# Optimization experiments

Measured on AMD Instinct MI355X. Metric: run time of the kernel, lower is better.

Reference implementation:

```python
import jax, jax.numpy as jnp
import numpy as np

N_POINTS = 1048576
N_LEVELS = 16
F = 2
BASE_RES = 16
FINEST_RES = 512
LOG2_HASH = 19
SIZES = [2 ** min(i + 1, LOG2_HASH) for i in range(N_LEVELS)]  # per-level table rows (powers of 2)
OFFS = np.concatenate([[0], np.cumsum(SIZES)]).astype(np.int64)  # static row offsets into packed table
TOTAL_ROWS = int(OFFS[-1])  # 131070
# hash primes from the torch module; uint32 wraparound matches int64 low-bit behavior
# because each table size is a power of two <= 2^19 < 2^32, so h % 2^k == low k bits.
P0, P1, P2, P3 = np.uint32(1), np.uint32(2654435761), np.uint32(29675113), np.uint32(123456789)
CORNERS = np.array([[0,0,0],[1,0,0],[0,1,0],[1,1,0],
                    [0,0,1],[1,0,1],[0,1,1],[1,1,1]], dtype=np.uint32)  # torch stacking order


def setup_inputs() -> dict:
    key = jax.random.key(0)
    k1, k2 = jax.random.split(key)
    coords = jax.random.uniform(k1, (N_POINTS, 3), dtype=jnp.float32, minval=-1.0, maxval=1.0)
    hash_init_scale = 0.001
    table = jax.random.uniform(k2, (TOTAL_ROWS, F), dtype=jnp.float32,
                               minval=-hash_init_scale, maxval=hash_init_scale)
    return {"coords": coords, "table": table}


def _encode(coords, table):
    corners = jnp.asarray(CORNERS)  # [8,3] uint32
    outs = []
    for level in range(N_LEVELS):
        res = min(BASE_RES * (2 ** level), FINEST_RES)
        cs = (coords + 1.0) * res           # [N,3]
        cf = jnp.floor(cs)
        frac = cs - cf                      # [N,3]
        base = cf.astype(jnp.uint32)        # coords >= -1 so floor >= 0
        c = base[None, :, :] + corners[:, None, :]   # [8,N,3]
        x, y, z = c[..., 0], c[..., 1], c[..., 2]
        h = x * P0
        h = h * P1 + y
        h = h * P2 + z
        h = h * P3
        h = (h & jnp.uint32(SIZES[level] - 1)).astype(jnp.int32)  # mod power-of-2 table size
        feats = table[int(OFFS[level]) + h]          # [8,N,F] gather
        tx = frac[..., 0:1]; ty = frac[..., 1:2]; tz = frac[..., 2:3]
        f = (feats[0] * (1 - tx) * (1 - ty) * (1 - tz)
             + feats[1] * tx * (1 - ty) * (1 - tz)
             + feats[2] * (1 - tx) * ty * (1 - tz)
             + feats[3] * tx * ty * (1 - tz)
             + feats[4] * (1 - tx) * (1 - ty) * tz
             + feats[5] * tx * (1 - ty) * tz
             + feats[6] * (1 - tx) * ty * tz
             + feats[7] * tx * ty * tz)              # [N,F]
        outs.append(f)
    return jnp.concatenate(outs, axis=-1)            # [N, N_LEVELS*F]


def reference(coords, table):
    return _encode(coords, table)
```

## Files before the change

### kernel.cpp

```cpp
#include <hip/hip_runtime.h>
#include <hip/hip_fp16.h>


#define N_POINTS 1048576
#define BLOCK 1024
#define STAGED_ROWS 16382
#define STAGED_BYTES (STAGED_ROWS * 4)

__device__ __forceinline__ float2 ldsRow(const unsigned* __restrict__ lds, unsigned idx) {
    unsigned u = lds[idx];
    __half2 h = *(__half2*)&u;
    return __half22float2(h);
}

__global__ __launch_bounds__(BLOCK, 8) void ngp_encode_kernel(
    const float* __restrict__ coords,
    const float* __restrict__ table,
    float* __restrict__ out)
{
    extern __shared__ unsigned lds_tb[];

    {
        const float4* __restrict__ t4 = (const float4*)table;
        uint2* __restrict__ l2 = (uint2*)lds_tb;
        const int n = STAGED_ROWS / 2;
        for (int r = threadIdx.x; r < n; r += BLOCK) {
            float4 v = t4[r];
            __half2 a = __floats2half2_rn(v.x, v.y);
            __half2 b = __floats2half2_rn(v.z, v.w);
            uint2 u;
            u.x = *(unsigned*)&a;
            u.y = *(unsigned*)&b;
            l2[r] = u;
        }
    }
    __syncthreads();

    const int i = blockIdx.x * BLOCK + threadIdx.x;

    const float px = coords[3 * i + 0];
    const float py = coords[3 * i + 1];
    const float pz = coords[3 * i + 2];

    constexpr unsigned P1 = 2654435761u, P2 = 29675113u, P3 = 123456789u;
    constexpr unsigned HA = P1 * P2 * P3;
    constexpr unsigned HB = P2 * P3;
    constexpr unsigned HC = P3;
    const unsigned D[8] = {0u, HA, HB, HA + HB, HC, HA + HC, HB + HC, HA + HB + HC};

    const float2* __restrict__ tb = (const float2*)table;

    float res_out[32];

#pragma unroll
    for (int l = 0; l < 5; ++l) {
        const float fres = (float)(16 << l);
        const float csx = (px + 1.0f) * fres;
        const float csy = (py + 1.0f) * fres;
        const float csz = (pz + 1.0f) * fres;
        const float cfx = floorf(csx), cfy = floorf(csy), cfz = floorf(csz);
        const float tx = csx - cfx, ty = csy - cfy, tz = csz - cfz;
        const unsigned h000 = (unsigned)cfx * HA + (unsigned)cfy * HB + (unsigned)cfz * HC;
        const float ux = 1.0f - tx, uy = 1.0f - ty, uz = 1.0f - tz;
        const float w[8] = {ux*uy*uz, tx*uy*uz, ux*ty*uz, tx*ty*uz,
                            ux*uy*tz, tx*uy*tz, ux*ty*tz, tx*ty*tz};
        const unsigned mask = (2u << l) - 1u;
        const unsigned off  = (2u << l) - 2u;
        float o0 = 0.0f, o1 = 0.0f;
#pragma unroll
        for (int c = 0; c < 8; ++c) {
            float2 f = ldsRow(lds_tb, off + ((h000 + D[c]) & mask));
            o0 += f.x * w[c];
            o1 += f.y * w[c];
        }
        res_out[2 * l + 0] = o0;
        res_out[2 * l + 1] = o1;
    }

    float w5[8];
    unsigned H[8];
    {
        const float fres = 512.0f;
        const float csx = (px + 1.0f) * fres;
        const float csy = (py + 1.0f) * fres;
        const float csz = (pz + 1.0f) * fres;
        const float cfx = floorf(csx), cfy = floorf(csy), cfz = floorf(csz);
        const float tx = csx - cfx, ty = csy - cfy, tz = csz - cfz;
        const unsigned h000 = (unsigned)cfx * HA + (unsigned)cfy * HB + (unsigned)cfz * HC;
        const float ux = 1.0f - tx, uy = 1.0f - ty, uz = 1.0f - tz;
        w5[0] = ux*uy*uz; w5[1] = tx*uy*uz; w5[2] = ux*ty*uz; w5[3] = tx*ty*uz;
        w5[4] = ux*uy*tz; w5[5] = tx*uy*tz; w5[6] = ux*ty*tz; w5[7] = tx*ty*tz;
#pragma unroll
        for (int c = 0; c < 8; ++c) H[c] = h000 + D[c];
    }

#pragma unroll
    for (int l = 5; l <= 12; ++l) {
        const unsigned mask = (2u << l) - 1u;
        const unsigned off  = (2u << l) - 2u;
        float o0 = 0.0f, o1 = 0.0f;
#pragma unroll
        for (int c = 0; c < 8; ++c) {
            float2 f = ldsRow(lds_tb, off + (H[c] & mask));
            o0 += f.x * w5[c];
            o1 += f.y * w5[c];
        }
        res_out[2 * l + 0] = o0;
        res_out[2 * l + 1] = o1;
    }

#pragma unroll
    for (int l = 13; l <= 15; ++l) {
        const unsigned mask = (2u << l) - 1u;
        const unsigned off  = (2u << l) - 2u;
        float o0 = 0.0f, o1 = 0.0f;
#pragma unroll
        for (int c = 0; c < 8; ++c) {
            float2 f = tb[off + (H[c] & mask)];
            o0 += f.x * w5[c];
            o1 += f.y * w5[c];
        }
        res_out[2 * l + 0] = o0;
        res_out[2 * l + 1] = o1;
    }

    float4* __restrict__ o4 = (float4*)(out + (size_t)i * 32);
#pragma unroll
    for (int k = 0; k < 8; ++k) {
        o4[k] = make_float4(res_out[4 * k + 0], res_out[4 * k + 1],
                            res_out[4 * k + 2], res_out[4 * k + 3]);
    }
}

extern "C" void kernel_launch(void* const* d_in, const int* in_sizes, int n_in,
                              void* d_out, int out_size, void* d_ws, size_t ws_size,
                              hipStream_t stream) {
    const float* coords = (const float*)d_in[0];
    const float* table  = (const float*)d_in[1];
    float* out = (float*)d_out;

    hipFuncSetAttribute((const void*)ngp_encode_kernel,
                        hipFuncAttributeMaxDynamicSharedMemorySize,
                        STAGED_BYTES);

    const int grid = N_POINTS / BLOCK;
    ngp_encode_kernel<<<grid, BLOCK, STAGED_BYTES, stream>>>(coords, table, out);
}
```

Before: 253.8 us.

## Split each point across 8 threads with two levels each in a persistent grid

Each point is now handled by 8 threads, each computing two hash levels and writing one float4, which gives coalesced output stores and lower per-thread register pressure. The grid becomes 512 persistent blocks that each loop over 16 chunks, so the LDS staging of the table happens once per block and is amortised over more work. LDS allocation is raised to 64KB, which limits occupancy, and coordinates are loaded redundantly by 8 threads. Divergence from the per-level resolution and LDS-versus-global branching within a wavefront also becomes possible.

```diff
diff --git a/kernel.cpp b/kernel.cpp
--- a/kernel.cpp
+++ b/kernel.cpp
@@ -4,8 +4,10 @@
 
 #define N_POINTS 1048576
 #define BLOCK 1024
+#define NBLOCKS 512
+#define ITERS 16
 #define STAGED_ROWS 16382
-#define STAGED_BYTES (STAGED_ROWS * 4)
+#define LDS_BYTES 65536
 
 __device__ __forceinline__ float2 ldsRow(const unsigned* __restrict__ lds, unsigned idx) {
     unsigned u = lds[idx];
@@ -13,7 +15,7 @@
     return __half22float2(h);
 }
 
-__global__ __launch_bounds__(BLOCK, 8) void ngp_encode_kernel(
+__global__ __launch_bounds__(BLOCK) void ngp_encode_kernel(
     const float* __restrict__ coords,
     const float* __restrict__ table,
     float* __restrict__ out)
@@ -36,12 +38,6 @@
     }
     __syncthreads();
 
-    const int i = blockIdx.x * BLOCK + threadIdx.x;
-
-    const float px = coords[3 * i + 0];
-    const float py = coords[3 * i + 1];
-    const float pz = coords[3 * i + 2];
-
     constexpr unsigned P1 = 2654435761u, P2 = 29675113u, P3 = 123456789u;
     constexpr unsigned HA = P1 * P2 * P3;
     constexpr unsigned HB = P2 * P3;
@@ -49,86 +45,61 @@
     const unsigned D[8] = {0u, HA, HB, HA + HB, HC, HA + HC, HB + HC, HA + HB + HC};
 
     const float2* __restrict__ tb = (const float2*)table;
+    float4* __restrict__ out4 = (float4*)out;
 
-    float res_out[32];
+    const int q = threadIdx.x & 7;
+
+    for (int it = 0; it < ITERS; ++it) {
+        const int t = (blockIdx.x * ITERS + it) * BLOCK + threadIdx.x;
+        const int p = t >> 3;
+
+        const float px = coords[3 * p + 0];
+        const float py = coords[3 * p + 1];
+        const float pz = coords[3 * p + 2];
+
+        float4 result;
+        float* rf = (float*)&result;
 
 #pragma unroll
-    for (int l = 0; l < 5; ++l) {
-        const float fres = (float)(16 << l);
-        const float csx = (px + 1.0f) * fres;
-        const float csy = (py + 1.0f) * fres;
-        const float csz = (pz + 1.0f) * fres;
-        const float cfx = floorf(csx), cfy = floorf(csy), cfz = floorf(csz);
-        const float tx = csx - cfx, ty = csy - cfy, tz = csz - cfz;
-        const unsigned h000 = (unsigned)cfx * HA + (unsigned)cfy * HB + (unsigned)cfz * HC;
-        const float ux = 1.0f - tx, uy = 1.0f - ty, uz = 1.0f - tz;
-        const float w[8] = {ux*uy*uz, tx*uy*uz, ux*ty*uz, tx*ty*uz,
-                            ux*uy*tz, tx*uy*tz, ux*ty*tz, tx*ty*tz};
-        const unsigned mask = (2u << l) - 1u;
-        const unsigned off  = (2u << l) - 2u;
-        float o0 = 0.0f, o1 = 0.0f;
+        for (int e = 0; e < 2; ++e) {
+            const int l = 2 * q + e;
+            const float fres = (l < 5) ? (float)(16 << l) : 512.0f;
+
+            const float csx = (px + 1.0f) * fres;
+            const float csy = (py + 1.0f) * fres;
+            const float csz = (pz + 1.0f) * fres;
+            const float cfx = floorf(csx), cfy = floorf(csy), cfz = floorf(csz);
+            const float tx = csx - cfx, ty = csy - cfy, tz = csz - cfz;
+            const unsigned h000 = (unsigned)cfx * HA + (unsigned)cfy * HB + (unsigned)cfz * HC;
+
+            const float ux = 1.0f - tx, uy = 1.0f - ty, uz = 1.0f - tz;
+            const float w[8] = {ux*uy*uz, tx*uy*uz, ux*ty*uz, tx*ty*uz,
+                                ux*uy*tz, tx*uy*tz, ux*ty*tz, tx*ty*tz};
+
+            const unsigned mask = (2u << l) - 1u;
+            const unsigned off  = (2u << l) - 2u;
+
+            float o0 = 0.0f, o1 = 0.0f;
+            if (l <= 12) {
 #pragma unroll
-        for (int c = 0; c < 8; ++c) {
-            float2 f = ldsRow(lds_tb, off + ((h000 + D[c]) & mask));
-            o0 += f.x * w[c];
-            o1 += f.y * w[c];
+                for (int c = 0; c < 8; ++c) {
+                    float2 f = ldsRow(lds_tb, off + ((h000 + D[c]) & mask));
+                    o0 += f.x * w[c];
+                    o1 += f.y * w[c];
+                }
+            } else {
+#pragma unroll
+                for (int c = 0; c < 8; ++c) {
+                    float2 f = tb[off + ((h000 + D[c]) & mask)];
+                    o0 += f.x * w[c];
+                    o1 += f.y * w[c];
+                }
+            }
+            rf[2 * e + 0] = o0;
+            rf[2 * e + 1] = o1;
         }
-        res_out[2 * l + 0] = o0;
-        res_out[2 * l + 1] = o1;
-    }
 
-    float w5[8];
-    unsigned H[8];
-    {
-        const float fres = 512.0f;
-        const float csx = (px + 1.0f) * fres;
-        const float csy = (py + 1.0f) * fres;
-        const float csz = (pz + 1.0f) * fres;
-        const float cfx = floorf(csx), cfy = floorf(csy), cfz = floorf(csz);
-        const float tx = csx - cfx, ty = csy - cfy, tz = csz - cfz;
-        const unsigned h000 = (unsigned)cfx * HA + (unsigned)cfy * HB + (unsigned)cfz * HC;
-        const float ux = 1.0f - tx, uy = 1.0f - ty, uz = 1.0f - tz;
-        w5[0] = ux*uy*uz; w5[1] = tx*uy*uz; w5[2] = ux*ty*uz; w5[3] = tx*ty*uz;
-        w5[4] = ux*uy*tz; w5[5] = tx*uy*tz; w5[6] = ux*ty*tz; w5[7] = tx*ty*tz;
-#pragma unroll
-        for (int c = 0; c < 8; ++c) H[c] = h000 + D[c];
-    }
-
-#pragma unroll
-    for (int l = 5; l <= 12; ++l) {
-        const unsigned mask = (2u << l) - 1u;
-        const unsigned off  = (2u << l) - 2u;
-        float o0 = 0.0f, o1 = 0.0f;
-#pragma unroll
-        for (int c = 0; c < 8; ++c) {
-            float2 f = ldsRow(lds_tb, off + (H[c] & mask));
-            o0 += f.x * w5[c];
-            o1 += f.y * w5[c];
-        }
-        res_out[2 * l + 0] = o0;
-        res_out[2 * l + 1] = o1;
-    }
-
-#pragma unroll
-    for (int l = 13; l <= 15; ++l) {
-        const unsigned mask = (2u << l) - 1u;
-        const unsigned off  = (2u << l) - 2u;
-        float o0 = 0.0f, o1 = 0.0f;
-#pragma unroll
-        for (int c = 0; c < 8; ++c) {
-            float2 f = tb[off + (H[c] & mask)];
-            o0 += f.x * w5[c];
-            o1 += f.y * w5[c];
-        }
-        res_out[2 * l + 0] = o0;
-        res_out[2 * l + 1] = o1;
-    }
-
-    float4* __restrict__ o4 = (float4*)(out + (size_t)i * 32);
-#pragma unroll
-    for (int k = 0; k < 8; ++k) {
-        o4[k] = make_float4(res_out[4 * k + 0], res_out[4 * k + 1],
-                            res_out[4 * k + 2], res_out[4 * k + 3]);
+        out4[t] = result;
     }
 }
 
@@ -141,8 +112,7 @@
 
     hipFuncSetAttribute((const void*)ngp_encode_kernel,
                         hipFuncAttributeMaxDynamicSharedMemorySize,
-                        STAGED_BYTES);
+                        LDS_BYTES);
 
-    const int grid = N_POINTS / BLOCK;
-    ngp_encode_kernel<<<grid, BLOCK, STAGED_BYTES, stream>>>(coords, table, out);
+    ngp_encode_kernel<<<NBLOCKS, BLOCK, LDS_BYTES, stream>>>(coords, table, out);
 }
```

Result: faster. 244.7 us (-3.6%).
